# Performance work log

Measured on AMD Instinct MI355X. Metric: run time of the kernel, lower is better.

The kernel has to match this reference:

```python
import jax, jax.numpy as jnp
import numpy as np

N = 16384      # batch of nodes
K = 25         # max_keep neighbors per node per relation (fixed sample)
R = 3          # number of outgoing relations from the source mode
D = 256        # feature dim (feat_dims)
OUT = 256      # out_dims
NTOT = 100000  # number of nodes in each mode's table
BAG = 8        # final EmbeddingBag mean bag size (offsets stride)


def setup_inputs() -> dict:
    key = jax.random.key(0)
    ks = jax.random.split(key, 7)
    nodes = jax.random.randint(ks[0], (N,), 0, NTOT)
    neigh_idx = jax.random.randint(ks[1], (R, N, K), 0, NTOT)
    table_self = jax.random.normal(ks[2], (NTOT, D), jnp.float32) * 0.02
    tables_to = jax.random.normal(ks[3], (R, NTOT, D), jnp.float32) * 0.02
    W_self = jax.random.normal(ks[4], (OUT, D), jnp.float32) * 0.05
    W_rel = jax.random.normal(ks[5], (R, OUT, D), jnp.float32) * 0.05
    W_comp = jax.random.normal(ks[6], (OUT, (R + 1) * OUT), jnp.float32) * 0.05
    return {"nodes": nodes, "neigh_idx": neigh_idx, "table_self": table_self,
            "tables_to": tables_to, "W_self": W_self, "W_rel": W_rel,
            "W_comp": W_comp}


def reference(nodes, neigh_idx, table_self, tables_to, W_self, W_rel, W_comp):
    # self features: features(nodes, mode, range(N)) -> [N, D]; self_params.mm
    self_feat = table_self[nodes] @ W_self.T                     # [N, OUT]
    # per-relation: gather sampled neighbors, EmbeddingBag-mean, relation matmul
    neigh_feats = []
    for r in range(R):  # small fixed relation count (structurally distinct params)
        nm = tables_to[r][neigh_idx[r]].mean(axis=1)             # [N, K, D] -> [N, D]
        neigh_feats.append(nm @ W_rel[r].T)                      # [N, OUT]
    # concat=True path: cat([rel_0, rel_1, rel_2, self]) then compress
    combined = jnp.concatenate(neigh_feats + [self_feat], axis=1)  # [N, (R+1)*OUT]
    h = jax.nn.relu(combined @ W_comp.T)                         # [N, OUT]
    # final EmbeddingBag mean over nodes with uniform offsets stride BAG
    return h.reshape(N // BAG, BAG, OUT).mean(axis=1)            # [N/BAG, OUT]
```

## Files before the change

kernel.cpp:

```cpp
#include <hip/hip_runtime.h>
#include <hip/hip_bf16.h>

#define NNODES 16384
#define KNEI 25
#define NREL 3
#define DIM 256
#define OUTD 256
#define NTOTAL 100000

typedef __attribute__((ext_vector_type(8))) short short8;
typedef __attribute__((ext_vector_type(4))) float f32x4;

static __device__ __forceinline__ unsigned short f2bf(float x) {
    union { float f; unsigned u; } v; v.f = x;
    unsigned r = v.u + 0x7fff + ((v.u >> 16) & 1);
    return (unsigned short)(r >> 16);
}

__global__ __launch_bounds__(256) void prep_M(
        const float* __restrict__ W_self,
        const float* __restrict__ W_rel,
        const float* __restrict__ W_comp,
        unsigned short* __restrict__ M) {
    const int slot = blockIdx.x >> 5;
    const int o0   = (blockIdx.x & 31) * 8;
    const int t    = threadIdx.x;
    const float* Wslot = (slot < NREL) ? (W_rel + (size_t)slot * OUTD * DIM)
                                       : W_self;
    float acc[8];
#pragma unroll
    for (int oi = 0; oi < 8; ++oi) acc[oi] = 0.f;
    for (int j = 0; j < 256; ++j) {
        const float wv = Wslot[j * 256 + t];
#pragma unroll
        for (int oi = 0; oi < 8; ++oi)
            acc[oi] += W_comp[(size_t)(o0 + oi) * 1024 + slot * 256 + j] * wv;
    }
#pragma unroll
    for (int oi = 0; oi < 8; ++oi)
        M[(size_t)(o0 + oi) * 1024 + slot * 256 + t] = f2bf(acc[oi]);
}

#define GSTRIDE 1032

__global__ __launch_bounds__(256, 4) void encoder_main(
        const int*   __restrict__ nodes,
        const int*   __restrict__ neigh_idx,
        const float* __restrict__ table_self,
        const float* __restrict__ tables_to,
        const unsigned short* __restrict__ M,
        float* __restrict__ out) {
    __shared__ unsigned short G[16 * GSTRIDE];

    const int tid  = threadIdx.x;
    const int wave = tid >> 6;
    const int lane = tid & 63;
    const int n0   = blockIdx.x * 16;

    {
        const int d4 = lane * 4;
        const float invK = 1.0f / (float)KNEI;
#pragma unroll
        for (int i = 0; i < 4; ++i) {
            const int li = wave * 4 + i;
            const int n  = n0 + li;
#pragma unroll
            for (int r = 0; r < NREL; ++r) {
                const int* idxp = neigh_idx + ((size_t)r * NNODES + n) * KNEI;
                const float* tab = tables_to + (size_t)r * NTOTAL * DIM;
                float4 acc = make_float4(0.f, 0.f, 0.f, 0.f);
#pragma unroll 5
                for (int j = 0; j < KNEI; ++j) {
                    const int idx = idxp[j];
                    const float4 v = *(const float4*)(tab + (size_t)idx * DIM + d4);
                    acc.x += v.x; acc.y += v.y; acc.z += v.z; acc.w += v.w;
                }
                ushort4 pk;
                pk.x = f2bf(acc.x * invK); pk.y = f2bf(acc.y * invK);
                pk.z = f2bf(acc.z * invK); pk.w = f2bf(acc.w * invK);
                *(ushort4*)&G[li * GSTRIDE + r * 256 + d4] = pk;
            }
            {
                const int row = nodes[n];
                const float4 v = *(const float4*)(table_self + (size_t)row * DIM + d4);
                ushort4 pk;
                pk.x = f2bf(v.x); pk.y = f2bf(v.y);
                pk.z = f2bf(v.z); pk.w = f2bf(v.w);
                *(ushort4*)&G[li * GSTRIDE + 3 * 256 + d4] = pk;
            }
        }
    }
    __syncthreads();

    const int quad = lane >> 4;
    const int l16  = lane & 15;
    f32x4 acc[4];
#pragma unroll
    for (int ct = 0; ct < 4; ++ct) acc[ct] = (f32x4){0.f, 0.f, 0.f, 0.f};

    for (int k0 = 0; k0 < 1024; k0 += 32) {
        const short8 a = *(const short8*)&G[l16 * GSTRIDE + k0 + quad * 8];
#pragma unroll
        for (int ct = 0; ct < 4; ++ct) {
            const int o = wave * 64 + ct * 16 + l16;
            const short8 b = *(const short8*)(M + (size_t)o * 1024 + k0 + quad * 8);
            acc[ct] = __builtin_amdgcn_mfma_f32_16x16x32_bf16(a, b, acc[ct], 0, 0, 0);
        }
    }

    const size_t orow0 = (size_t)blockIdx.x * 2;
#pragma unroll
    for (int ct = 0; ct < 4; ++ct) {
        float s = fmaxf(acc[ct][0], 0.f) + fmaxf(acc[ct][1], 0.f)
                + fmaxf(acc[ct][2], 0.f) + fmaxf(acc[ct][3], 0.f);
        s += __shfl_xor(s, 16, 64);
        s *= 0.125f;
        const int col = wave * 64 + ct * 16 + l16;
        if (quad == 0)      out[orow0 * 256 + col]       = s;
        else if (quad == 2) out[(orow0 + 1) * 256 + col] = s;
    }
}

extern "C" void kernel_launch(void* const* d_in, const int* in_sizes, int n_in,
                              void* d_out, int out_size, void* d_ws, size_t ws_size,
                              hipStream_t stream) {
    const int*   nodes  = (const int*)  d_in[0];
    const int*   neigh  = (const int*)  d_in[1];
    const float* tself  = (const float*)d_in[2];
    const float* tto    = (const float*)d_in[3];
    const float* wself  = (const float*)d_in[4];
    const float* wrel   = (const float*)d_in[5];
    const float* wcomp  = (const float*)d_in[6];
    float* outp = (float*)d_out;
    unsigned short* M = (unsigned short*)d_ws;

    prep_M<<<128, 256, 0, stream>>>(wself, wrel, wcomp, M);
    encoder_main<<<1024, 256, 0, stream>>>(nodes, neigh, tself, tto, M, outp);
}
```

Baseline: 645.8 us.

## Split fused encoder into separate gather and GEMM kernels via workspace buffer

Splits the gather-then-GEMM kernel into a gather kernel with one block per (relation, 16-node tile), which writes bf16 features to a global workspace buffer, and a separate GEMM kernel that reloads them into shared memory. The gather now keeps five independent accumulators so more row loads are in flight at once. prep_M stages its W_comp slice in shared memory and uses twice as many blocks. This adds a 32 MB global round trip and an extra launch in exchange for more parallelism and memory-level concurrency in the gather, and falls back to the old fused kernel if the workspace is too small.

```diff
diff --git a/kernel.cpp b/kernel.cpp
--- a/kernel.cpp
+++ b/kernel.cpp
@@ -22,26 +22,140 @@
         const float* __restrict__ W_rel,
         const float* __restrict__ W_comp,
         unsigned short* __restrict__ M) {
-    const int slot = blockIdx.x >> 5;
-    const int o0   = (blockIdx.x & 31) * 8;
+    const int slot = blockIdx.x >> 6;
+    const int o0   = (blockIdx.x & 63) * 4;
     const int t    = threadIdx.x;
-    const float* Wslot = (slot < NREL) ? (W_rel + (size_t)slot * OUTD * DIM)
-                                       : W_self;
-    float acc[8];
-#pragma unroll
-    for (int oi = 0; oi < 8; ++oi) acc[oi] = 0.f;
-    for (int j = 0; j < 256; ++j) {
-        const float wv = Wslot[j * 256 + t];
-#pragma unroll
-        for (int oi = 0; oi < 8; ++oi)
-            acc[oi] += W_comp[(size_t)(o0 + oi) * 1024 + slot * 256 + j] * wv;
-    }
-#pragma unroll
-    for (int oi = 0; oi < 8; ++oi)
+    const float* __restrict__ Wslot = (slot < NREL)
+        ? (W_rel + (size_t)slot * OUTD * DIM) : W_self;
+    __shared__ float C[4 * 256];
+#pragma unroll
+    for (int oi = 0; oi < 4; ++oi)
+        C[oi * 256 + t] = W_comp[(size_t)(o0 + oi) * 1024 + slot * 256 + t];
+    __syncthreads();
+    float acc[4] = {0.f, 0.f, 0.f, 0.f};
+    for (int j = 0; j < 256; j += 8) {
+#pragma unroll
+        for (int u = 0; u < 8; ++u) {
+            const float wv = Wslot[(size_t)(j + u) * 256 + t];
+#pragma unroll
+            for (int oi = 0; oi < 4; ++oi)
+                acc[oi] += C[oi * 256 + j + u] * wv;
+        }
+    }
+#pragma unroll
+    for (int oi = 0; oi < 4; ++oi)
         M[(size_t)(o0 + oi) * 1024 + slot * 256 + t] = f2bf(acc[oi]);
 }
 
+__global__ __launch_bounds__(256) void gather_kernel(
+        const int*   __restrict__ nodes,
+        const int*   __restrict__ neigh_idx,
+        const float* __restrict__ table_self,
+        const float* __restrict__ tables_to,
+        unsigned short* __restrict__ G) {
+    const int b    = blockIdx.x;
+    const int r    = b >> 10;
+    const int blk  = b & 1023;
+    const int wave = threadIdx.x >> 6;
+    const int lane = threadIdx.x & 63;
+    const int d4   = lane * 4;
+
+    if (r < NREL) {
+        const float* __restrict__ tab = tables_to + (size_t)r * NTOTAL * DIM;
+        const float invK = 1.0f / (float)KNEI;
+#pragma unroll
+        for (int i = 0; i < 4; ++i) {
+            const int n = blk * 16 + wave * 4 + i;
+            const int* idxp = neigh_idx + ((size_t)r * NNODES + n) * KNEI;
+            float4 acc[5];
+#pragma unroll
+            for (int j = 0; j < 5; ++j)
+                acc[j] = *(const float4*)(tab + (size_t)idxp[j] * DIM + d4);
+#pragma unroll
+            for (int g = 1; g < 5; ++g) {
+#pragma unroll
+                for (int j = 0; j < 5; ++j) {
+                    const float4 v =
+                        *(const float4*)(tab + (size_t)idxp[g * 5 + j] * DIM + d4);
+                    acc[j].x += v.x; acc[j].y += v.y;
+                    acc[j].z += v.z; acc[j].w += v.w;
+                }
+            }
+            float4 s;
+            s.x = (acc[0].x + acc[1].x) + (acc[2].x + acc[3].x) + acc[4].x;
+            s.y = (acc[0].y + acc[1].y) + (acc[2].y + acc[3].y) + acc[4].y;
+            s.z = (acc[0].z + acc[1].z) + (acc[2].z + acc[3].z) + acc[4].z;
+            s.w = (acc[0].w + acc[1].w) + (acc[2].w + acc[3].w) + acc[4].w;
+            ushort4 pk;
+            pk.x = f2bf(s.x * invK); pk.y = f2bf(s.y * invK);
+            pk.z = f2bf(s.z * invK); pk.w = f2bf(s.w * invK);
+            *(ushort4*)(G + (size_t)n * 1024 + r * 256 + d4) = pk;
+        }
+    } else {
+#pragma unroll
+        for (int i = 0; i < 4; ++i) {
+            const int n = blk * 16 + wave * 4 + i;
+            const float4 v =
+                *(const float4*)(table_self + (size_t)nodes[n] * DIM + d4);
+            ushort4 pk;
+            pk.x = f2bf(v.x); pk.y = f2bf(v.y);
+            pk.z = f2bf(v.z); pk.w = f2bf(v.w);
+            *(ushort4*)(G + (size_t)n * 1024 + 3 * 256 + d4) = pk;
+        }
+    }
+}
+
 #define GSTRIDE 1032
+
+__global__ __launch_bounds__(256, 4) void gemm_kernel(
+        const unsigned short* __restrict__ G,
+        const unsigned short* __restrict__ M,
+        float* __restrict__ out) {
+    __shared__ unsigned short A[16 * GSTRIDE];
+
+    const int t    = threadIdx.x;
+    const int wave = t >> 6;
+    const int lane = t & 63;
+    const int quad = lane >> 4;
+    const int l16  = lane & 15;
+
+    const unsigned short* gsrc = G + (size_t)blockIdx.x * 16 * 1024;
+#pragma unroll
+    for (int rnd = 0; rnd < 8; ++rnd) {
+        const int l   = rnd * 2048 + t * 8;
+        const int row = l >> 10;
+        const int col = l & 1023;
+        *(short8*)&A[row * GSTRIDE + col] = *(const short8*)(gsrc + l);
+    }
+    __syncthreads();
+
+    f32x4 acc[4];
+#pragma unroll
+    for (int ct = 0; ct < 4; ++ct) acc[ct] = (f32x4){0.f, 0.f, 0.f, 0.f};
+
+    for (int k0 = 0; k0 < 1024; k0 += 32) {
+        const short8 a = *(const short8*)&A[l16 * GSTRIDE + k0 + quad * 8];
+#pragma unroll
+        for (int ct = 0; ct < 4; ++ct) {
+            const int o = wave * 64 + ct * 16 + l16;
+            const short8 bfrag =
+                *(const short8*)(M + (size_t)o * 1024 + k0 + quad * 8);
+            acc[ct] = __builtin_amdgcn_mfma_f32_16x16x32_bf16(a, bfrag, acc[ct], 0, 0, 0);
+        }
+    }
+
+    const size_t orow0 = (size_t)blockIdx.x * 2;
+#pragma unroll
+    for (int ct = 0; ct < 4; ++ct) {
+        float s = fmaxf(acc[ct][0], 0.f) + fmaxf(acc[ct][1], 0.f)
+                + fmaxf(acc[ct][2], 0.f) + fmaxf(acc[ct][3], 0.f);
+        s += __shfl_xor(s, 16, 64);
+        s *= 0.125f;
+        const int col = wave * 64 + ct * 16 + l16;
+        if (quad == 0)      out[orow0 * 256 + col]       = s;
+        else if (quad == 2) out[(orow0 + 1) * 256 + col] = s;
+    }
+}
 
 __global__ __launch_bounds__(256, 4) void encoder_main(
         const int*   __restrict__ nodes,
@@ -50,13 +164,11 @@
         const float* __restrict__ tables_to,
         const unsigned short* __restrict__ M,
         float* __restrict__ out) {
-    __shared__ unsigned short G[16 * GSTRIDE];
-
+    __shared__ unsigned short Gt[16 * GSTRIDE];
     const int tid  = threadIdx.x;
     const int wave = tid >> 6;
     const int lane = tid & 63;
     const int n0   = blockIdx.x * 16;
-
     {
         const int d4 = lane * 4;
         const float invK = 1.0f / (float)KNEI;
@@ -71,35 +183,31 @@
                 float4 acc = make_float4(0.f, 0.f, 0.f, 0.f);
 #pragma unroll 5
                 for (int j = 0; j < KNEI; ++j) {
-                    const int idx = idxp[j];
-                    const float4 v = *(const float4*)(tab + (size_t)idx * DIM + d4);
+                    const float4 v = *(const float4*)(tab + (size_t)idxp[j] * DIM + d4);
                     acc.x += v.x; acc.y += v.y; acc.z += v.z; acc.w += v.w;
                 }
                 ushort4 pk;
                 pk.x = f2bf(acc.x * invK); pk.y = f2bf(acc.y * invK);
                 pk.z = f2bf(acc.z * invK); pk.w = f2bf(acc.w * invK);
-                *(ushort4*)&G[li * GSTRIDE + r * 256 + d4] = pk;
+                *(ushort4*)&Gt[li * GSTRIDE + r * 256 + d4] = pk;
             }
             {
-                const int row = nodes[n];
-                const float4 v = *(const float4*)(table_self + (size_t)row * DIM + d4);
+                const float4 v = *(const float4*)(table_self + (size_t)nodes[n] * DIM + d4);
                 ushort4 pk;
                 pk.x = f2bf(v.x); pk.y = f2bf(v.y);
                 pk.z = f2bf(v.z); pk.w = f2bf(v.w);
-                *(ushort4*)&G[li * GSTRIDE + 3 * 256 + d4] = pk;
+                *(ushort4*)&Gt[li * GSTRIDE + 3 * 256 + d4] = pk;
             }
         }
     }
     __syncthreads();
-
     const int quad = lane >> 4;
     const int l16  = lane & 15;
     f32x4 acc[4];
 #pragma unroll
     for (int ct = 0; ct < 4; ++ct) acc[ct] = (f32x4){0.f, 0.f, 0.f, 0.f};
-
     for (int k0 = 0; k0 < 1024; k0 += 32) {
-        const short8 a = *(const short8*)&G[l16 * GSTRIDE + k0 + quad * 8];
+        const short8 a = *(const short8*)&Gt[l16 * GSTRIDE + k0 + quad * 8];
 #pragma unroll
         for (int ct = 0; ct < 4; ++ct) {
             const int o = wave * 64 + ct * 16 + l16;
@@ -107,7 +215,6 @@
             acc[ct] = __builtin_amdgcn_mfma_f32_16x16x32_bf16(a, b, acc[ct], 0, 0, 0);
         }
     }
-
     const size_t orow0 = (size_t)blockIdx.x * 2;
 #pragma unroll
     for (int ct = 0; ct < 4; ++ct) {
@@ -132,8 +239,16 @@
     const float* wrel   = (const float*)d_in[5];
     const float* wcomp  = (const float*)d_in[6];
     float* outp = (float*)d_out;
+
     unsigned short* M = (unsigned short*)d_ws;
-
-    prep_M<<<128, 256, 0, stream>>>(wself, wrel, wcomp, M);
-    encoder_main<<<1024, 256, 0, stream>>>(nodes, neigh, tself, tto, M, outp);
-}
+    const size_t g_off  = 1u << 20;
+    const size_t g_size = (size_t)NNODES * 1024 * 2;
+    prep_M<<<256, 256, 0, stream>>>(wself, wrel, wcomp, M);
+    if (ws_size >= g_off + g_size) {
+        unsigned short* G = (unsigned short*)((char*)d_ws + g_off);
+        gather_kernel<<<4096, 256, 0, stream>>>(nodes, neigh, tself, tto, G);
+        gemm_kernel<<<1024, 256, 0, stream>>>(G, M, outp);
+    } else {
+        encoder_main<<<1024, 256, 0, stream>>>(nodes, neigh, tself, tto, M, outp);
+    }
+}
```

Result: faster. 615.5 us (-4.7%).
